# Optimization experiments

Measured on AMD Instinct MI355X. Metric: run time of the kernel, lower is better.

## Reference

```python
import jax, jax.numpy as jnp
import numpy as np

GROUPS = 3
EPS = 1e-5


def grouped_conv1x1(x, w, groups):
    # x: [B, Cin, H, W], w: [Cout, Cin//groups] (1x1 kernel flattened)
    B, Cin, H, W = x.shape
    Cout = w.shape[0]
    xg = x.reshape(B, groups, Cin // groups, H, W)
    wg = w.reshape(groups, Cout // groups, Cin // groups)
    yg = jnp.einsum('bgihw,goi->bgohw', xg, wg)
    return yg.reshape(B, Cout, H, W)


def depthwise_conv3x3(x, w):
    # x: [B, C, H, W], w: [C, 1, 3, 3]; stride 1, padding 1
    C = x.shape[1]
    return jax.lax.conv_general_dilated(
        x, w, window_strides=(1, 1), padding=((1, 1), (1, 1)),
        dimension_numbers=('NCHW', 'OIHW', 'NCHW'), feature_group_count=C)


def batchnorm(x, gamma, beta, mean, var):
    inv = gamma * jax.lax.rsqrt(var + EPS)
    return x * inv[None, :, None, None] + (beta - mean * inv)[None, :, None, None]


def channel_shuffle(x, groups):
    B, C, H, W = x.shape
    return x.reshape(B, groups, C // groups, H, W).transpose(0, 2, 1, 3, 4).reshape(B, C, H, W)


def setup_inputs() -> dict:
    key = jax.random.key(0)
    ks = jax.random.split(key, 12)
    B, Cin, H, W = 32, 240, 56, 56
    Cout = 240
    mid = Cout // 4  # 60
    inp = {
        'x': jax.random.normal(ks[0], (B, Cin, H, W), jnp.float32),
        'w1': jax.random.normal(ks[1], (mid, Cin // GROUPS), jnp.float32) * 0.05,
        'g1': jax.random.normal(ks[2], (mid,), jnp.float32) * 0.1 + 1.0,
        'b1': jax.random.normal(ks[3], (mid,), jnp.float32) * 0.1,
        'm1': jax.random.normal(ks[4], (mid,), jnp.float32) * 0.1,
        'v1': jax.random.uniform(ks[5], (mid,), jnp.float32, 0.5, 1.5),
        'w2': jax.random.normal(ks[6], (mid, 1, 3, 3), jnp.float32) * 0.1,
        'g2': jnp.ones((mid,), jnp.float32),
        'b2': jnp.zeros((mid,), jnp.float32),
        'm2': jax.random.normal(ks[7], (mid,), jnp.float32) * 0.1,
        'v2': jax.random.uniform(ks[8], (mid,), jnp.float32, 0.5, 1.5),
        'w3': jax.random.normal(ks[9], (Cout, mid // GROUPS), jnp.float32) * 0.05,
        'g3': jax.random.normal(ks[10], (Cout,), jnp.float32) * 0.1 + 1.0,
        'b3': jnp.zeros((Cout,), jnp.float32),
        'm3': jax.random.normal(ks[11], (Cout,), jnp.float32) * 0.1,
        'v3': jnp.ones((Cout,), jnp.float32),
    }
    return inp


def reference(x, w1, g1, b1, m1, v1, w2, g2, b2, m2, v2, w3, g3, b3, m3, v3):
    out = grouped_conv1x1(x, w1, GROUPS)
    out = jax.nn.relu(batchnorm(out, g1, b1, m1, v1))
    out = depthwise_conv3x3(out, w2)
    out = batchnorm(out, g2, b2, m2, v2)
    out = channel_shuffle(out, GROUPS)
    out = grouped_conv1x1(out, w3, GROUPS)
    out = jax.nn.relu(batchnorm(out, g3, b3, m3, v3))
    # in_channels == out_channels -> identity shortcut
    return out + x
```

## Files before the change

kernel.cpp:

```cpp
#include <hip/hip_runtime.h>
#include <hip/hip_bf16.h>

#define HH 56
#define WW 56
#define HWSZ 3136
#define NB 32
#define CIN 240
#define MID 60
#define NG 3
#define CING 80
#define MIDG 20
#define COUT 240
#define COUTG 80
#define BN_EPS 1e-5f

__global__ __launch_bounds__(256) void k1_conv1_bn_relu(
        const float* __restrict__ x, const float* __restrict__ w1,
        const float* __restrict__ g1, const float* __restrict__ b1,
        const float* __restrict__ m1, const float* __restrict__ v1,
        float* __restrict__ t1) {
    __shared__ float wlds[MID * CING];
    __shared__ float s1[MID], sh1[MID];
    const int tid = threadIdx.x;
    for (int i = tid; i < MID * CING; i += 256) wlds[i] = w1[i];
    if (tid < MID) {
        float inv = g1[tid] * rsqrtf(v1[tid] + BN_EPS);
        s1[tid] = inv;
        sh1[tid] = b1[tid] - m1[tid] * inv;
    }
    __syncthreads();

    const int item = blockIdx.x * 256 + tid;
    const unsigned q  = (unsigned)item & 3u;
    const unsigned pg = (unsigned)item >> 2;
    const unsigned p4 = pg % 784u;
    const unsigned bg = pg / 784u;
    const unsigned b = bg / 3u, g = bg % 3u;
    const int pos = (int)p4 * 4;

    const float4* xb = (const float4*)(x + ((size_t)(b * CIN + g * CING)) * HWSZ) + p4;
    float4 acc[5];
#pragma unroll
    for (int c = 0; c < 5; c++) acc[c] = make_float4(0.f, 0.f, 0.f, 0.f);

    const float4* wl4 = (const float4*)wlds;
#pragma unroll 5
    for (int c4 = 0; c4 < CING / 4; c4++) {
        float4 xv0 = xb[(c4 * 4 + 0) * 784];
        float4 xv1 = xb[(c4 * 4 + 1) * 784];
        float4 xv2 = xb[(c4 * 4 + 2) * 784];
        float4 xv3 = xb[(c4 * 4 + 3) * 784];
#pragma unroll
        for (int co = 0; co < 5; co++) {
            float4 wv = wl4[(g * MIDG + q * 5 + co) * (CING / 4) + c4];
            acc[co].x += wv.x * xv0.x + wv.y * xv1.x + wv.z * xv2.x + wv.w * xv3.x;
            acc[co].y += wv.x * xv0.y + wv.y * xv1.y + wv.z * xv2.y + wv.w * xv3.y;
            acc[co].z += wv.x * xv0.z + wv.y * xv1.z + wv.z * xv2.z + wv.w * xv3.z;
            acc[co].w += wv.x * xv0.w + wv.y * xv1.w + wv.z * xv2.w + wv.w * xv3.w;
        }
    }

#pragma unroll
    for (int co = 0; co < 5; co++) {
        int ch = g * MIDG + q * 5 + co;
        float sc = s1[ch], sf = sh1[ch];
        float4 o;
        o.x = fmaxf(acc[co].x * sc + sf, 0.f);
        o.y = fmaxf(acc[co].y * sc + sf, 0.f);
        o.z = fmaxf(acc[co].z * sc + sf, 0.f);
        o.w = fmaxf(acc[co].w * sc + sf, 0.f);
        *(float4*)(t1 + ((size_t)(b * MID + ch)) * HWSZ + pos) = o;
    }
}

__global__ __launch_bounds__(256) void k2_dw_bn(
        const float* __restrict__ t1, const float* __restrict__ w2,
        const float* __restrict__ g2, const float* __restrict__ b2,
        const float* __restrict__ m2, const float* __restrict__ v2,
        float* __restrict__ t2) {
    const int item = blockIdx.x * 256 + threadIdx.x;
    const unsigned bc = (unsigned)item / 784u;
    const unsigned p4 = (unsigned)item % 784u;
    const unsigned c = bc % (unsigned)MID;
    const int pos = (int)p4 * 4;
    const int h = pos / WW;
    const int w = pos % WW;

    const float* base = t1 + (size_t)bc * HWSZ;
    float k[9];
#pragma unroll
    for (int i = 0; i < 9; i++) k[i] = w2[c * 9 + i];

    float acc0 = 0.f, acc1 = 0.f, acc2 = 0.f, acc3 = 0.f;
#pragma unroll
    for (int dy = -1; dy <= 1; dy++) {
        int r = h + dy;
        if (r < 0 || r >= HH) continue;
        const float* row = base + r * WW + w;
        float4 mid4 = *(const float4*)row;
        float v0 = (w > 0) ? row[-1] : 0.f;
        float v5 = (w + 4 < WW) ? row[4] : 0.f;
        float va[6] = {v0, mid4.x, mid4.y, mid4.z, mid4.w, v5};
        const float k0 = k[(dy + 1) * 3 + 0];
        const float k1 = k[(dy + 1) * 3 + 1];
        const float k2 = k[(dy + 1) * 3 + 2];
        acc0 += k0 * va[0] + k1 * va[1] + k2 * va[2];
        acc1 += k0 * va[1] + k1 * va[2] + k2 * va[3];
        acc2 += k0 * va[2] + k1 * va[3] + k2 * va[4];
        acc3 += k0 * va[3] + k1 * va[4] + k2 * va[5];
    }

    float inv = g2[c] * rsqrtf(v2[c] + BN_EPS);
    float sf = b2[c] - m2[c] * inv;
    float4 o;
    o.x = acc0 * inv + sf;
    o.y = acc1 * inv + sf;
    o.z = acc2 * inv + sf;
    o.w = acc3 * inv + sf;
    *(float4*)(t2 + (size_t)bc * HWSZ + pos) = o;
}

__global__ __launch_bounds__(256) void k3_shuffle_conv_bn_relu_res(
        const float* __restrict__ t2, const float* __restrict__ w3,
        const float* __restrict__ g3, const float* __restrict__ b3,
        const float* __restrict__ m3, const float* __restrict__ v3,
        const float* __restrict__ x, float* __restrict__ out) {
    __shared__ float wT[NG * MIDG * COUTG];
    __shared__ float s3[COUT], sh3[COUT];
    const int tid = threadIdx.x;
    for (int i = tid; i < NG * MIDG * COUTG; i += 256) {
        int co_glob = i / MIDG;
        int ci = i % MIDG;
        int gg = co_glob / COUTG;
        int cg = co_glob % COUTG;
        wT[(gg * MIDG + ci) * COUTG + cg] = w3[i];
    }
    if (tid < COUT) {
        float inv = g3[tid] * rsqrtf(v3[tid] + BN_EPS);
        s3[tid] = inv;
        sh3[tid] = b3[tid] - m3[tid] * inv;
    }
    __syncthreads();

    const int item = blockIdx.x * 256 + tid;
    const unsigned q  = (unsigned)item & 3u;
    const unsigned pg = (unsigned)item >> 2;
    const unsigned p4 = pg % 784u;
    const unsigned bg = pg / 784u;
    const unsigned b = bg / 3u, g = bg % 3u;
    const int pos = (int)p4 * 4;

    float4 acc[MIDG];
#pragma unroll
    for (int c = 0; c < MIDG; c++) acc[c] = make_float4(0.f, 0.f, 0.f, 0.f);

    const float4* wl4 = (const float4*)wT;
#pragma unroll 4
    for (int ci = 0; ci < MIDG; ci++) {
        int csh = (int)g * MIDG + ci;
        int c2 = (csh % 3) * 20 + csh / 3;
        float4 xv = *(const float4*)(t2 + ((size_t)(b * MID + c2)) * HWSZ + pos);
        int wbase = ((g * MIDG + ci) * COUTG + q * MIDG) / 4;
#pragma unroll
        for (int k4 = 0; k4 < 5; k4++) {
            float4 wv = wl4[wbase + k4];
            acc[k4 * 4 + 0].x += wv.x * xv.x; acc[k4 * 4 + 0].y += wv.x * xv.y;
            acc[k4 * 4 + 0].z += wv.x * xv.z; acc[k4 * 4 + 0].w += wv.x * xv.w;
            acc[k4 * 4 + 1].x += wv.y * xv.x; acc[k4 * 4 + 1].y += wv.y * xv.y;
            acc[k4 * 4 + 1].z += wv.y * xv.z; acc[k4 * 4 + 1].w += wv.y * xv.w;
            acc[k4 * 4 + 2].x += wv.z * xv.x; acc[k4 * 4 + 2].y += wv.z * xv.y;
            acc[k4 * 4 + 2].z += wv.z * xv.z; acc[k4 * 4 + 2].w += wv.z * xv.w;
            acc[k4 * 4 + 3].x += wv.w * xv.x; acc[k4 * 4 + 3].y += wv.w * xv.y;
            acc[k4 * 4 + 3].z += wv.w * xv.z; acc[k4 * 4 + 3].w += wv.w * xv.w;
        }
    }

#pragma unroll
    for (int co = 0; co < MIDG; co++) {
        int cg = (int)g * COUTG + (int)q * MIDG + co;
        float sc = s3[cg], sf = sh3[cg];
        float4 xr = *(const float4*)(x + ((size_t)(b * CIN + cg)) * HWSZ + pos);
        float4 o;
        o.x = fmaxf(acc[co].x * sc + sf, 0.f) + xr.x;
        o.y = fmaxf(acc[co].y * sc + sf, 0.f) + xr.y;
        o.z = fmaxf(acc[co].z * sc + sf, 0.f) + xr.z;
        o.w = fmaxf(acc[co].w * sc + sf, 0.f) + xr.w;
        *(float4*)(out + ((size_t)(b * COUT + cg)) * HWSZ + pos) = o;
    }
}

extern "C" void kernel_launch(void* const* d_in, const int* in_sizes, int n_in,
                              void* d_out, int out_size, void* d_ws, size_t ws_size,
                              hipStream_t stream) {
    const float* x  = (const float*)d_in[0];
    const float* w1 = (const float*)d_in[1];
    const float* g1 = (const float*)d_in[2];
    const float* b1 = (const float*)d_in[3];
    const float* m1 = (const float*)d_in[4];
    const float* v1 = (const float*)d_in[5];
    const float* w2 = (const float*)d_in[6];
    const float* g2 = (const float*)d_in[7];
    const float* b2 = (const float*)d_in[8];
    const float* m2 = (const float*)d_in[9];
    const float* v2 = (const float*)d_in[10];
    const float* w3 = (const float*)d_in[11];
    const float* g3 = (const float*)d_in[12];
    const float* b3 = (const float*)d_in[13];
    const float* m3 = (const float*)d_in[14];
    const float* v3 = (const float*)d_in[15];
    float* out = (float*)d_out;

    float* t1 = (float*)d_ws;
    float* t2 = t1 + (size_t)NB * MID * HWSZ;

    k1_conv1_bn_relu<<<1176, 256, 0, stream>>>(x, w1, g1, b1, m1, v1, t1);
    k2_dw_bn<<<5880, 256, 0, stream>>>(t1, w2, g2, b2, m2, v2, t2);
    k3_shuffle_conv_bn_relu_res<<<1176, 256, 0, stream>>>(t2, w3, g3, b3, m3, v3, x, out);
}
```

Baseline: 89.06 us.

## Fuse grouped 1x1 conv and depthwise 3x3 into one row-tiled kernel

Merges the first grouped 1x1 conv + BN + ReLU with the depthwise 3x3 + BN into one kernel. Each block computes a 9-row halo tile of 20 mid channels into LDS and then runs the depthwise stencil from LDS, which removes the t1 round trip through global memory and one launch. It also folds the BN scales into the weights and writes t2 in shuffled channel order, so the last kernel reads channels contiguously. The cost is recomputing two halo rows per 7-row tile and a larger LDS footprint, which may lower occupancy.

```diff
diff --git a/kernel.cpp b/kernel.cpp
--- a/kernel.cpp
+++ b/kernel.cpp
@@ -1,32 +1,150 @@
 #include <hip/hip_runtime.h>
-#include <hip/hip_bf16.h>
-
-#define HH 56
+
+#define BN_EPS 1e-5f
 #define WW 56
 #define HWSZ 3136
 #define NB 32
 #define CIN 240
 #define MID 60
-#define NG 3
-#define CING 80
 #define MIDG 20
 #define COUT 240
 #define COUTG 80
-#define BN_EPS 1e-5f
-
-__global__ __launch_bounds__(256) void k1_conv1_bn_relu(
-        const float* __restrict__ x, const float* __restrict__ w1,
-        const float* __restrict__ g1, const float* __restrict__ b1,
-        const float* __restrict__ m1, const float* __restrict__ v1,
-        float* __restrict__ t1) {
-    __shared__ float wlds[MID * CING];
-    __shared__ float s1[MID], sh1[MID];
+#define TH 7
+#define THH 9
+
+__global__ __launch_bounds__(512, 2) void kA_conv1_dw(
+        const float* __restrict__ x,
+        const float* __restrict__ w1, const float* __restrict__ g1,
+        const float* __restrict__ b1, const float* __restrict__ m1,
+        const float* __restrict__ v1,
+        const float* __restrict__ w2, const float* __restrict__ g2,
+        const float* __restrict__ b2, const float* __restrict__ m2,
+        const float* __restrict__ v2,
+        float* __restrict__ t2) {
+    __shared__ float mid[MIDG * THH * WW];
+    __shared__ float w1s[MIDG * 80];
+    __shared__ float w2s[MIDG * 9];
+    __shared__ float shA[MIDG], shB[MIDG];
+
     const int tid = threadIdx.x;
-    for (int i = tid; i < MID * CING; i += 256) wlds[i] = w1[i];
-    if (tid < MID) {
-        float inv = g1[tid] * rsqrtf(v1[tid] + BN_EPS);
-        s1[tid] = inv;
-        sh1[tid] = b1[tid] - m1[tid] * inv;
+    const int bid = blockIdx.x;
+    const int t   = bid & 7;
+    const int gb  = bid >> 3;
+    const int g   = gb % 3;
+    const int b   = gb / 3;
+    const int h0  = t * TH;
+
+    for (int i = tid; i < MIDG * 80; i += 512) {
+        int chg = g * MIDG + i / 80;
+        w1s[i] = w1[chg * 80 + i % 80] * (g1[chg] * rsqrtf(v1[chg] + BN_EPS));
+    }
+    for (int i = tid; i < MIDG * 9; i += 512) {
+        int chg = g * MIDG + i / 9;
+        w2s[i] = w2[chg * 9 + i % 9] * (g2[chg] * rsqrtf(v2[chg] + BN_EPS));
+    }
+    if (tid < MIDG) {
+        int chg = g * MIDG + tid;
+        float s1v = g1[chg] * rsqrtf(v1[chg] + BN_EPS);
+        shA[tid] = b1[chg] - m1[chg] * s1v;
+        float s2v = g2[chg] * rsqrtf(v2[chg] + BN_EPS);
+        shB[tid] = b2[chg] - m2[chg] * s2v;
+    }
+    __syncthreads();
+
+    {
+        const int q   = tid & 3;
+        const int idx = tid >> 2;
+        if (idx < 126) {
+            const int r  = idx / 14, c4 = idx % 14;
+            const int hh = h0 - 1 + r;
+            float4 acc[5];
+#pragma unroll
+            for (int c = 0; c < 5; c++) acc[c] = make_float4(0.f, 0.f, 0.f, 0.f);
+            if (hh >= 0 && hh < 56) {
+                const float* xp = x + ((size_t)(b * CIN + g * 80)) * HWSZ + hh * WW + c4 * 4;
+                const float4* w4 = (const float4*)w1s;
+#pragma unroll 4
+                for (int ci4 = 0; ci4 < 20; ci4++) {
+                    float4 xv0 = *(const float4*)(xp + (ci4 * 4 + 0) * HWSZ);
+                    float4 xv1 = *(const float4*)(xp + (ci4 * 4 + 1) * HWSZ);
+                    float4 xv2 = *(const float4*)(xp + (ci4 * 4 + 2) * HWSZ);
+                    float4 xv3 = *(const float4*)(xp + (ci4 * 4 + 3) * HWSZ);
+#pragma unroll
+                    for (int c = 0; c < 5; c++) {
+                        float4 wv = w4[(q * 5 + c) * 20 + ci4];
+                        acc[c].x += wv.x * xv0.x + wv.y * xv1.x + wv.z * xv2.x + wv.w * xv3.x;
+                        acc[c].y += wv.x * xv0.y + wv.y * xv1.y + wv.z * xv2.y + wv.w * xv3.y;
+                        acc[c].z += wv.x * xv0.z + wv.y * xv1.z + wv.z * xv2.z + wv.w * xv3.z;
+                        acc[c].w += wv.x * xv0.w + wv.y * xv1.w + wv.z * xv2.w + wv.w * xv3.w;
+                    }
+                }
+#pragma unroll
+                for (int c = 0; c < 5; c++) {
+                    float s = shA[q * 5 + c];
+                    acc[c].x = fmaxf(acc[c].x + s, 0.f);
+                    acc[c].y = fmaxf(acc[c].y + s, 0.f);
+                    acc[c].z = fmaxf(acc[c].z + s, 0.f);
+                    acc[c].w = fmaxf(acc[c].w + s, 0.f);
+                }
+            }
+#pragma unroll
+            for (int c = 0; c < 5; c++)
+                *(float4*)(mid + ((q * 5 + c) * THH + r) * WW + c4 * 4) = acc[c];
+        }
+    }
+    __syncthreads();
+
+#pragma unroll
+    for (int k = 0; k < 4; k++) {
+        const int it = tid + k * 512;
+        if (it < MIDG * 98) {
+            const int ch = it / 98;
+            const int pq = it % 98;
+            const int r = pq / 14, c4 = pq % 14;
+            const float* base = mid + ch * (THH * WW);
+            const float* kw = w2s + ch * 9;
+            float4 a = make_float4(0.f, 0.f, 0.f, 0.f);
+#pragma unroll
+            for (int dy = 0; dy < 3; dy++) {
+                const float* row = base + (r + dy) * WW + c4 * 4;
+                float4 m = *(const float4*)row;
+                float l  = (c4 > 0)  ? row[-1] : 0.f;
+                float rt = (c4 < 13) ? row[4]  : 0.f;
+                const float k0 = kw[dy * 3 + 0];
+                const float k1 = kw[dy * 3 + 1];
+                const float k2 = kw[dy * 3 + 2];
+                a.x += k0 * l   + k1 * m.x + k2 * m.y;
+                a.y += k0 * m.x + k1 * m.y + k2 * m.z;
+                a.z += k0 * m.y + k1 * m.z + k2 * m.w;
+                a.w += k0 * m.z + k1 * m.w + k2 * rt;
+            }
+            const float s = shB[ch];
+            a.x += s; a.y += s; a.z += s; a.w += s;
+            const int jj = ch * 3 + g;
+            *(float4*)(t2 + ((size_t)(b * MID + jj)) * HWSZ + (h0 + r) * WW + c4 * 4) = a;
+        }
+    }
+}
+
+__global__ __launch_bounds__(256) void kB_conv3_res(
+        const float* __restrict__ t2, const float* __restrict__ w3,
+        const float* __restrict__ g3, const float* __restrict__ b3,
+        const float* __restrict__ m3, const float* __restrict__ v3,
+        const float* __restrict__ x, float* __restrict__ out) {
+    __shared__ float wT[3 * MIDG * COUTG];
+    __shared__ float s3[COUT], sh3[COUT];
+    const int tid = threadIdx.x;
+    for (int i = tid; i < 3 * MIDG * COUTG; i += 256) {
+        int co_glob = i / MIDG;
+        int ci = i % MIDG;
+        int gg = co_glob / COUTG;
+        int cg = co_glob % COUTG;
+        wT[(gg * MIDG + ci) * COUTG + cg] = w3[i];
+    }
+    if (tid < COUT) {
+        float inv = g3[tid] * rsqrtf(v3[tid] + BN_EPS);
+        s3[tid] = inv;
+        sh3[tid] = b3[tid] - m3[tid] * inv;
     }
     __syncthreads();
 
@@ -38,118 +156,6 @@
     const unsigned b = bg / 3u, g = bg % 3u;
     const int pos = (int)p4 * 4;
 
-    const float4* xb = (const float4*)(x + ((size_t)(b * CIN + g * CING)) * HWSZ) + p4;
-    float4 acc[5];
-#pragma unroll
-    for (int c = 0; c < 5; c++) acc[c] = make_float4(0.f, 0.f, 0.f, 0.f);
-
-    const float4* wl4 = (const float4*)wlds;
-#pragma unroll 5
-    for (int c4 = 0; c4 < CING / 4; c4++) {
-        float4 xv0 = xb[(c4 * 4 + 0) * 784];
-        float4 xv1 = xb[(c4 * 4 + 1) * 784];
-        float4 xv2 = xb[(c4 * 4 + 2) * 784];
-        float4 xv3 = xb[(c4 * 4 + 3) * 784];
-#pragma unroll
-        for (int co = 0; co < 5; co++) {
-            float4 wv = wl4[(g * MIDG + q * 5 + co) * (CING / 4) + c4];
-            acc[co].x += wv.x * xv0.x + wv.y * xv1.x + wv.z * xv2.x + wv.w * xv3.x;
-            acc[co].y += wv.x * xv0.y + wv.y * xv1.y + wv.z * xv2.y + wv.w * xv3.y;
-            acc[co].z += wv.x * xv0.z + wv.y * xv1.z + wv.z * xv2.z + wv.w * xv3.z;
-            acc[co].w += wv.x * xv0.w + wv.y * xv1.w + wv.z * xv2.w + wv.w * xv3.w;
-        }
-    }
-
-#pragma unroll
-    for (int co = 0; co < 5; co++) {
-        int ch = g * MIDG + q * 5 + co;
-        float sc = s1[ch], sf = sh1[ch];
-        float4 o;
-        o.x = fmaxf(acc[co].x * sc + sf, 0.f);
-        o.y = fmaxf(acc[co].y * sc + sf, 0.f);
-        o.z = fmaxf(acc[co].z * sc + sf, 0.f);
-        o.w = fmaxf(acc[co].w * sc + sf, 0.f);
-        *(float4*)(t1 + ((size_t)(b * MID + ch)) * HWSZ + pos) = o;
-    }
-}
-
-__global__ __launch_bounds__(256) void k2_dw_bn(
-        const float* __restrict__ t1, const float* __restrict__ w2,
-        const float* __restrict__ g2, const float* __restrict__ b2,
-        const float* __restrict__ m2, const float* __restrict__ v2,
-        float* __restrict__ t2) {
-    const int item = blockIdx.x * 256 + threadIdx.x;
-    const unsigned bc = (unsigned)item / 784u;
-    const unsigned p4 = (unsigned)item % 784u;
-    const unsigned c = bc % (unsigned)MID;
-    const int pos = (int)p4 * 4;
-    const int h = pos / WW;
-    const int w = pos % WW;
-
-    const float* base = t1 + (size_t)bc * HWSZ;
-    float k[9];
-#pragma unroll
-    for (int i = 0; i < 9; i++) k[i] = w2[c * 9 + i];
-
-    float acc0 = 0.f, acc1 = 0.f, acc2 = 0.f, acc3 = 0.f;
-#pragma unroll
-    for (int dy = -1; dy <= 1; dy++) {
-        int r = h + dy;
-        if (r < 0 || r >= HH) continue;
-        const float* row = base + r * WW + w;
-        float4 mid4 = *(const float4*)row;
-        float v0 = (w > 0) ? row[-1] : 0.f;
-        float v5 = (w + 4 < WW) ? row[4] : 0.f;
-        float va[6] = {v0, mid4.x, mid4.y, mid4.z, mid4.w, v5};
-        const float k0 = k[(dy + 1) * 3 + 0];
-        const float k1 = k[(dy + 1) * 3 + 1];
-        const float k2 = k[(dy + 1) * 3 + 2];
-        acc0 += k0 * va[0] + k1 * va[1] + k2 * va[2];
-        acc1 += k0 * va[1] + k1 * va[2] + k2 * va[3];
-        acc2 += k0 * va[2] + k1 * va[3] + k2 * va[4];
-        acc3 += k0 * va[3] + k1 * va[4] + k2 * va[5];
-    }
-
-    float inv = g2[c] * rsqrtf(v2[c] + BN_EPS);
-    float sf = b2[c] - m2[c] * inv;
-    float4 o;
-    o.x = acc0 * inv + sf;
-    o.y = acc1 * inv + sf;
-    o.z = acc2 * inv + sf;
-    o.w = acc3 * inv + sf;
-    *(float4*)(t2 + (size_t)bc * HWSZ + pos) = o;
-}
-
-__global__ __launch_bounds__(256) void k3_shuffle_conv_bn_relu_res(
-        const float* __restrict__ t2, const float* __restrict__ w3,
-        const float* __restrict__ g3, const float* __restrict__ b3,
-        const float* __restrict__ m3, const float* __restrict__ v3,
-        const float* __restrict__ x, float* __restrict__ out) {
-    __shared__ float wT[NG * MIDG * COUTG];
-    __shared__ float s3[COUT], sh3[COUT];
-    const int tid = threadIdx.x;
-    for (int i = tid; i < NG * MIDG * COUTG; i += 256) {
-        int co_glob = i / MIDG;
-        int ci = i % MIDG;
-        int gg = co_glob / COUTG;
-        int cg = co_glob % COUTG;
-        wT[(gg * MIDG + ci) * COUTG + cg] = w3[i];
-    }
-    if (tid < COUT) {
-        float inv = g3[tid] * rsqrtf(v3[tid] + BN_EPS);
-        s3[tid] = inv;
-        sh3[tid] = b3[tid] - m3[tid] * inv;
-    }
-    __syncthreads();
-
-    const int item = blockIdx.x * 256 + tid;
-    const unsigned q  = (unsigned)item & 3u;
-    const unsigned pg = (unsigned)item >> 2;
-    const unsigned p4 = pg % 784u;
-    const unsigned bg = pg / 784u;
-    const unsigned b = bg / 3u, g = bg % 3u;
-    const int pos = (int)p4 * 4;
-
     float4 acc[MIDG];
 #pragma unroll
     for (int c = 0; c < MIDG; c++) acc[c] = make_float4(0.f, 0.f, 0.f, 0.f);
@@ -158,9 +164,8 @@
 #pragma unroll 4
     for (int ci = 0; ci < MIDG; ci++) {
         int csh = (int)g * MIDG + ci;
-        int c2 = (csh % 3) * 20 + csh / 3;
-        float4 xv = *(const float4*)(t2 + ((size_t)(b * MID + c2)) * HWSZ + pos);
-        int wbase = ((g * MIDG + ci) * COUTG + q * MIDG) / 4;
+        float4 xv = *(const float4*)(t2 + ((size_t)(b * MID + csh)) * HWSZ + pos);
+        int wbase = (csh * COUTG + q * MIDG) / 4;
 #pragma unroll
         for (int k4 = 0; k4 < 5; k4++) {
             float4 wv = wl4[wbase + k4];
@@ -210,10 +215,9 @@
     const float* v3 = (const float*)d_in[15];
     float* out = (float*)d_out;
 
-    float* t1 = (float*)d_ws;
-    float* t2 = t1 + (size_t)NB * MID * HWSZ;
-
-    k1_conv1_bn_relu<<<1176, 256, 0, stream>>>(x, w1, g1, b1, m1, v1, t1);
-    k2_dw_bn<<<5880, 256, 0, stream>>>(t1, w2, g2, b2, m2, v2, t2);
-    k3_shuffle_conv_bn_relu_res<<<1176, 256, 0, stream>>>(t2, w3, g3, b3, m3, v3, x, out);
+    float* t2 = (float*)d_ws;
+
+    kA_conv1_dw<<<768, 512, 0, stream>>>(x, w1, g1, b1, m1, v1,
+                                         w2, g2, b2, m2, v2, t2);
+    kB_conv3_res<<<1176, 256, 0, stream>>>(t2, w3, g3, b3, m3, v3, x, out);
 }
```

Measured after the change: 84.16 us. 5.5% less time.

## Split conv1 input channels across lanes with shuffle reduction; fold BN scales into weights

Applied to the files above, without the earlier changes.

Conv1 is restructured so each of four lanes reads a distinct quarter of the input channels (20 each) and accumulates all 20 outputs, then the partial sums are reduced with cross-lane shuffles. Before, every lane re-read all 80 channels. The BN scales of conv1 and the depthwise conv are folded into their weights. The channel shuffle moves from the conv3 gather into the depthwise kernel's store index. The cost is more accumulator registers, 20 float4, which can lower occupancy, plus the shuffle-reduction overhead.

```diff
diff --git a/kernel.cpp b/kernel.cpp
--- a/kernel.cpp
+++ b/kernel.cpp
@@ -1,79 +1,93 @@
 #include <hip/hip_runtime.h>
-#include <hip/hip_bf16.h>
-
-#define HH 56
+
+#define BN_EPS 1e-5f
 #define WW 56
 #define HWSZ 3136
 #define NB 32
 #define CIN 240
 #define MID 60
-#define NG 3
-#define CING 80
 #define MIDG 20
 #define COUT 240
 #define COUTG 80
-#define BN_EPS 1e-5f
-
-__global__ __launch_bounds__(256) void k1_conv1_bn_relu(
+
+__global__ __launch_bounds__(256, 4) void k1_conv1_bn_relu(
         const float* __restrict__ x, const float* __restrict__ w1,
         const float* __restrict__ g1, const float* __restrict__ b1,
         const float* __restrict__ m1, const float* __restrict__ v1,
         float* __restrict__ t1) {
-    __shared__ float wlds[MID * CING];
-    __shared__ float s1[MID], sh1[MID];
+    __shared__ float wT[3 * 80 * MIDG];
+    __shared__ float sh1L[MID];
     const int tid = threadIdx.x;
-    for (int i = tid; i < MID * CING; i += 256) wlds[i] = w1[i];
+    for (int i = tid; i < MID * 80; i += 256) {
+        int co_glob = i / 80;
+        int ci = i % 80;
+        int gg = co_glob / MIDG, co = co_glob % MIDG;
+        float s1v = g1[co_glob] * rsqrtf(v1[co_glob] + BN_EPS);
+        wT[(gg * 80 + ci) * MIDG + co] = w1[i] * s1v;
+    }
     if (tid < MID) {
-        float inv = g1[tid] * rsqrtf(v1[tid] + BN_EPS);
-        s1[tid] = inv;
-        sh1[tid] = b1[tid] - m1[tid] * inv;
+        float s1v = g1[tid] * rsqrtf(v1[tid] + BN_EPS);
+        sh1L[tid] = b1[tid] - m1[tid] * s1v;
     }
     __syncthreads();
 
-    const int item = blockIdx.x * 256 + tid;
-    const unsigned q  = (unsigned)item & 3u;
-    const unsigned pg = (unsigned)item >> 2;
-    const unsigned p4 = pg % 784u;
-    const unsigned bg = pg / 784u;
-    const unsigned b = bg / 3u, g = bg % 3u;
-    const int pos = (int)p4 * 4;
-
-    const float4* xb = (const float4*)(x + ((size_t)(b * CIN + g * CING)) * HWSZ) + p4;
-    float4 acc[5];
-#pragma unroll
-    for (int c = 0; c < 5; c++) acc[c] = make_float4(0.f, 0.f, 0.f, 0.f);
-
-    const float4* wl4 = (const float4*)wlds;
-#pragma unroll 5
-    for (int c4 = 0; c4 < CING / 4; c4++) {
-        float4 xv0 = xb[(c4 * 4 + 0) * 784];
-        float4 xv1 = xb[(c4 * 4 + 1) * 784];
-        float4 xv2 = xb[(c4 * 4 + 2) * 784];
-        float4 xv3 = xb[(c4 * 4 + 3) * 784];
-#pragma unroll
-        for (int co = 0; co < 5; co++) {
-            float4 wv = wl4[(g * MIDG + q * 5 + co) * (CING / 4) + c4];
-            acc[co].x += wv.x * xv0.x + wv.y * xv1.x + wv.z * xv2.x + wv.w * xv3.x;
-            acc[co].y += wv.x * xv0.y + wv.y * xv1.y + wv.z * xv2.y + wv.w * xv3.y;
-            acc[co].z += wv.x * xv0.z + wv.y * xv1.z + wv.z * xv2.z + wv.w * xv3.z;
-            acc[co].w += wv.x * xv0.w + wv.y * xv1.w + wv.z * xv2.w + wv.w * xv3.w;
+    const int item  = blockIdx.x * 256 + tid;
+    const int chunk = item & 3;
+    const int pg    = item >> 2;
+    const int p4    = pg % 784;
+    const int bg    = pg / 784;
+    const int b = bg / 3, g = bg % 3;
+    const int pos = p4 * 4;
+
+    const float* xp = x + ((size_t)(b * CIN + g * 80 + chunk * 20)) * HWSZ + pos;
+    const float* wbase = wT + (g * 80 + chunk * 20) * MIDG;
+
+    float4 acc[MIDG];
+#pragma unroll
+    for (int j = 0; j < MIDG; j++) acc[j] = make_float4(0.f, 0.f, 0.f, 0.f);
+
+#pragma unroll 4
+    for (int ci = 0; ci < 20; ci++) {
+        float4 xv = *(const float4*)(xp + (size_t)ci * HWSZ);
+        const float4* wrow = (const float4*)(wbase + ci * MIDG);
+#pragma unroll
+        for (int k4 = 0; k4 < 5; k4++) {
+            float4 wv = wrow[k4];
+            acc[k4 * 4 + 0].x += wv.x * xv.x; acc[k4 * 4 + 0].y += wv.x * xv.y;
+            acc[k4 * 4 + 0].z += wv.x * xv.z; acc[k4 * 4 + 0].w += wv.x * xv.w;
+            acc[k4 * 4 + 1].x += wv.y * xv.x; acc[k4 * 4 + 1].y += wv.y * xv.y;
+            acc[k4 * 4 + 1].z += wv.y * xv.z; acc[k4 * 4 + 1].w += wv.y * xv.w;
+            acc[k4 * 4 + 2].x += wv.z * xv.x; acc[k4 * 4 + 2].y += wv.z * xv.y;
+            acc[k4 * 4 + 2].z += wv.z * xv.z; acc[k4 * 4 + 2].w += wv.z * xv.w;
+            acc[k4 * 4 + 3].x += wv.w * xv.x; acc[k4 * 4 + 3].y += wv.w * xv.y;
+            acc[k4 * 4 + 3].z += wv.w * xv.z; acc[k4 * 4 + 3].w += wv.w * xv.w;
         }
     }
 
 #pragma unroll
-    for (int co = 0; co < 5; co++) {
-        int ch = g * MIDG + q * 5 + co;
-        float sc = s1[ch], sf = sh1[ch];
-        float4 o;
-        o.x = fmaxf(acc[co].x * sc + sf, 0.f);
-        o.y = fmaxf(acc[co].y * sc + sf, 0.f);
-        o.z = fmaxf(acc[co].z * sc + sf, 0.f);
-        o.w = fmaxf(acc[co].w * sc + sf, 0.f);
-        *(float4*)(t1 + ((size_t)(b * MID + ch)) * HWSZ + pos) = o;
-    }
-}
-
-__global__ __launch_bounds__(256) void k2_dw_bn(
+    for (int j = 0; j < MIDG; j++) {
+        acc[j].x += __shfl_xor(acc[j].x, 1); acc[j].y += __shfl_xor(acc[j].y, 1);
+        acc[j].z += __shfl_xor(acc[j].z, 1); acc[j].w += __shfl_xor(acc[j].w, 1);
+        acc[j].x += __shfl_xor(acc[j].x, 2); acc[j].y += __shfl_xor(acc[j].y, 2);
+        acc[j].z += __shfl_xor(acc[j].z, 2); acc[j].w += __shfl_xor(acc[j].w, 2);
+    }
+
+#pragma unroll
+    for (int j = 0; j < MIDG; j++) {
+        if (j / 5 == chunk) {
+            int ch = g * MIDG + j;
+            float sf = sh1L[ch];
+            float4 o;
+            o.x = fmaxf(acc[j].x + sf, 0.f);
+            o.y = fmaxf(acc[j].y + sf, 0.f);
+            o.z = fmaxf(acc[j].z + sf, 0.f);
+            o.w = fmaxf(acc[j].w + sf, 0.f);
+            *(float4*)(t1 + ((size_t)(b * MID + ch)) * HWSZ + pos) = o;
+        }
+    }
+}
+
+__global__ __launch_bounds__(256) void k2_dw_bn_shuffle(
         const float* __restrict__ t1, const float* __restrict__ w2,
         const float* __restrict__ g2, const float* __restrict__ b2,
         const float* __restrict__ m2, const float* __restrict__ v2,
@@ -82,53 +96,51 @@
     const unsigned bc = (unsigned)item / 784u;
     const unsigned p4 = (unsigned)item % 784u;
     const unsigned c = bc % (unsigned)MID;
+    const unsigned b = bc / (unsigned)MID;
     const int pos = (int)p4 * 4;
     const int h = pos / WW;
     const int w = pos % WW;
 
+    const float inv = g2[c] * rsqrtf(v2[c] + BN_EPS);
+    const float sf  = b2[c] - m2[c] * inv;
     const float* base = t1 + (size_t)bc * HWSZ;
-    float k[9];
-#pragma unroll
-    for (int i = 0; i < 9; i++) k[i] = w2[c * 9 + i];
+    float kf[9];
+#pragma unroll
+    for (int i = 0; i < 9; i++) kf[i] = w2[c * 9 + i] * inv;
 
     float acc0 = 0.f, acc1 = 0.f, acc2 = 0.f, acc3 = 0.f;
 #pragma unroll
     for (int dy = -1; dy <= 1; dy++) {
         int r = h + dy;
-        if (r < 0 || r >= HH) continue;
+        if (r < 0 || r >= 56) continue;
         const float* row = base + r * WW + w;
         float4 mid4 = *(const float4*)row;
         float v0 = (w > 0) ? row[-1] : 0.f;
         float v5 = (w + 4 < WW) ? row[4] : 0.f;
-        float va[6] = {v0, mid4.x, mid4.y, mid4.z, mid4.w, v5};
-        const float k0 = k[(dy + 1) * 3 + 0];
-        const float k1 = k[(dy + 1) * 3 + 1];
-        const float k2 = k[(dy + 1) * 3 + 2];
-        acc0 += k0 * va[0] + k1 * va[1] + k2 * va[2];
-        acc1 += k0 * va[1] + k1 * va[2] + k2 * va[3];
-        acc2 += k0 * va[2] + k1 * va[3] + k2 * va[4];
-        acc3 += k0 * va[3] + k1 * va[4] + k2 * va[5];
-    }
-
-    float inv = g2[c] * rsqrtf(v2[c] + BN_EPS);
-    float sf = b2[c] - m2[c] * inv;
+        const float k0 = kf[(dy + 1) * 3 + 0];
+        const float k1 = kf[(dy + 1) * 3 + 1];
+        const float k2 = kf[(dy + 1) * 3 + 2];
+        acc0 += k0 * v0     + k1 * mid4.x + k2 * mid4.y;
+        acc1 += k0 * mid4.x + k1 * mid4.y + k2 * mid4.z;
+        acc2 += k0 * mid4.y + k1 * mid4.z + k2 * mid4.w;
+        acc3 += k0 * mid4.z + k1 * mid4.w + k2 * v5;
+    }
+
     float4 o;
-    o.x = acc0 * inv + sf;
-    o.y = acc1 * inv + sf;
-    o.z = acc2 * inv + sf;
-    o.w = acc3 * inv + sf;
-    *(float4*)(t2 + (size_t)bc * HWSZ + pos) = o;
-}
-
-__global__ __launch_bounds__(256) void k3_shuffle_conv_bn_relu_res(
+    o.x = acc0 + sf; o.y = acc1 + sf; o.z = acc2 + sf; o.w = acc3 + sf;
+    const unsigned jj = (c % 20u) * 3u + c / 20u;
+    *(float4*)(t2 + ((size_t)(b * MID + jj)) * HWSZ + pos) = o;
+}
+
+__global__ __launch_bounds__(256) void kB_conv3_res(
         const float* __restrict__ t2, const float* __restrict__ w3,
         const float* __restrict__ g3, const float* __restrict__ b3,
         const float* __restrict__ m3, const float* __restrict__ v3,
         const float* __restrict__ x, float* __restrict__ out) {
-    __shared__ float wT[NG * MIDG * COUTG];
+    __shared__ float wT[3 * MIDG * COUTG];
     __shared__ float s3[COUT], sh3[COUT];
     const int tid = threadIdx.x;
-    for (int i = tid; i < NG * MIDG * COUTG; i += 256) {
+    for (int i = tid; i < 3 * MIDG * COUTG; i += 256) {
         int co_glob = i / MIDG;
         int ci = i % MIDG;
         int gg = co_glob / COUTG;
@@ -158,9 +170,8 @@
 #pragma unroll 4
     for (int ci = 0; ci < MIDG; ci++) {
         int csh = (int)g * MIDG + ci;
-        int c2 = (csh % 3) * 20 + csh / 3;
-        float4 xv = *(const float4*)(t2 + ((size_t)(b * MID + c2)) * HWSZ + pos);
-        int wbase = ((g * MIDG + ci) * COUTG + q * MIDG) / 4;
+        float4 xv = *(const float4*)(t2 + ((size_t)(b * MID + csh)) * HWSZ + pos);
+        int wbase = (csh * COUTG + q * MIDG) / 4;
 #pragma unroll
         for (int k4 = 0; k4 < 5; k4++) {
             float4 wv = wl4[wbase + k4];
@@ -185,7 +196,7 @@
         o.y = fmaxf(acc[co].y * sc + sf, 0.f) + xr.y;
         o.z = fmaxf(acc[co].z * sc + sf, 0.f) + xr.z;
         o.w = fmaxf(acc[co].w * sc + sf, 0.f) + xr.w;
-        *(float4*)(out + ((size_t)(b * COUT + cg)) * HWSZ + pos) = o;
+        *(float4*)(out + ((size_t)(b * CIN + cg)) * HWSZ + pos) = o;
     }
 }
 
@@ -214,6 +225,6 @@
     float* t2 = t1 + (size_t)NB * MID * HWSZ;
 
     k1_conv1_bn_relu<<<1176, 256, 0, stream>>>(x, w1, g1, b1, m1, v1, t1);
-    k2_dw_bn<<<5880, 256, 0, stream>>>(t1, w2, g2, b2, m2, v2, t2);
-    k3_shuffle_conv_bn_relu_res<<<1176, 256, 0, stream>>>(t2, w3, g3, b3, m3, v3, x, out);
-}
+    k2_dw_bn_shuffle<<<5880, 256, 0, stream>>>(t1, w2, g2, b2, m2, v2, t2);
+    kB_conv3_res<<<1176, 256, 0, stream>>>(t2, w3, g3, b3, m3, v3, x, out);
+}
```

Result: slower. 199.8 us (+124.4%).
